# Optimization experiments

Measured on AMD Instinct MI355X. Metric: run time of the kernel, lower is better.

## Reference

```python
import jax, jax.numpy as jnp
import numpy as np

B, S, E, H, SHARE = 32, 1024, 256, 256, 2


def setup_inputs() -> dict:
    key = jax.random.key(0)
    ks = jax.random.split(key, 14)
    sc_e = 1.0 / np.sqrt(E)
    sc_h = 1.0 / np.sqrt(H)
    mk = lambda k, shape, sc: (jax.random.normal(k, shape, jnp.float32) * sc)
    return {
        "inputs": jax.random.normal(ks[0], (B, S, E), jnp.float32),
        "mask": jnp.ones((B, S), jnp.float32),
        # forward-direction cell params
        "Wx": mk(ks[1], (E, 4 * H), sc_e),
        "Wh": mk(ks[2], (H, 4 * H), sc_h),
        "Ws": mk(ks[3], (H, 4 * H), sc_h),
        "b": jnp.zeros((4 * H,), jnp.float32),
        "Wrx": mk(ks[4], (SHARE, E, H), sc_e),
        "Wrh": mk(ks[5], (SHARE, H, H), sc_h),
        "br": jnp.zeros((SHARE, H), jnp.float32),
        # reverse-direction cell params (deepcopy in torch; distinct draws here)
        "Wx_r": mk(ks[6], (E, 4 * H), sc_e),
        "Wh_r": mk(ks[7], (H, 4 * H), sc_h),
        "Ws_r": mk(ks[8], (H, 4 * H), sc_h),
        "b_r": jnp.zeros((4 * H,), jnp.float32),
        "Wrx_r": mk(ks[9], (SHARE, E, H), sc_e),
        "Wrh_r": mk(ks[10], (SHARE, H, H), sc_h),
        "br_r": jnp.zeros((SHARE, H), jnp.float32),
        "idx": 1,
    }


def _run_dir(xs, ms, params, idx, reverse):
    # xs: [S,B,E] time-major, ms: [S,B]
    Wx, Wh, Ws, b, Wrx, Wrh, br = params
    if reverse:
        xs = xs[::-1]
        ms = ms[::-1]
    Bt = xs.shape[1]
    Hd = Wh.shape[0]
    K = Wrx.shape[0]
    h0 = jnp.zeros((Bt, Hd), xs.dtype)
    c0 = jnp.zeros((Bt, Hd), xs.dtype)
    s0 = jnp.zeros((K, Bt, Hd), xs.dtype)  # shared cells (init_s)

    def step(carry, xm):
        h, c, s = carry
        x_t, m_t = xm
        # gates read x, h, and the idx-selected shared cell
        z = x_t @ Wx + h @ Wh + s[idx] @ Ws + b  # [B, 4H]
        i, f, g, o = jnp.split(z, 4, axis=-1)
        c_new = jax.nn.sigmoid(f) * c + jax.nn.sigmoid(i) * jnp.tanh(g)
        h_new = jax.nn.sigmoid(o) * jnp.tanh(c_new)
        m = m_t[:, None]
        h = m * h_new + (1.0 - m) * h
        c = m * c_new + (1.0 - m) * c
        # shared-cell gates, all K at once: [K,B,H]
        r = jax.nn.sigmoid(
            jnp.einsum("be,keh->kbh", x_t, Wrx)
            + jnp.einsum("bh,khj->kbj", h, Wrh)
            + br[:, None, :]
        )
        s_new = r * s + (1.0 - r) * c[None]
        s = m[None] * s_new + (1.0 - m[None]) * s
        return (h, c, s), (h, c, s)

    _, (hs, cs, ss) = jax.lax.scan(step, (h0, c0, s0), (xs, ms))
    if reverse:
        hs, cs, ss = hs[::-1], cs[::-1], ss[::-1]
    return hs, cs, ss  # [S,B,H], [S,B,H], [S,K,B,H]


def reference(inputs, mask, Wx, Wh, Ws, b, Wrx, Wrh, br,
              Wx_r, Wh_r, Ws_r, b_r, Wrx_r, Wrh_r, br_r, idx):
    xs = inputs.transpose(1, 0, 2)  # [S,B,E]
    ms = mask.T  # [S,B]
    hs_f, cs_f, ss_f = _run_dir(xs, ms, (Wx, Wh, Ws, b, Wrx, Wrh, br), idx, False)
    hs_r, cs_r, ss_r = _run_dir(xs, ms, (Wx_r, Wh_r, Ws_r, b_r, Wrx_r, Wrh_r, br_r), idx, True)
    h_f = jnp.concatenate([hs_f, hs_r], axis=-1)  # [S,B,2H]
    c_f = jnp.concatenate([cs_f, cs_r], axis=-1)  # [S,B,2H]
    # final_list: per shared-cell index, stacked over time -> [K,S,B,2H]
    s_f = jnp.concatenate([ss_f, ss_r], axis=-1).transpose(1, 0, 2, 3)
    return (h_f, c_f, s_f)
```

## Files before the change

### kernel.cpp

```cpp
#include <hip/hip_runtime.h>
#include <hip/hip_bf16.h>
#include <cstdint>
#include <cstddef>


typedef __bf16 bf16x8 __attribute__((ext_vector_type(8)));
typedef float  f32x4  __attribute__((ext_vector_type(4)));
typedef unsigned long long u64x2 __attribute__((ext_vector_type(2)));

#define DEVINL __device__ __forceinline__

constexpr int Ss = 1024;

constexpr size_t OFF_FLAGS = 0;
constexpr size_t OFF_H   = 1024;
constexpr size_t SZ_HS   = (size_t)2*2*32*512;
constexpr size_t OFF_S   = OFF_H + SZ_HS;
constexpr size_t OFF_WH  = OFF_S + SZ_HS;
constexpr size_t SZ_W    = (size_t)2*1024*256*2;
constexpr size_t OFF_WX  = OFF_WH + SZ_W;
constexpr size_t OFF_WS  = OFF_WX + SZ_W;
constexpr size_t OFF_WRX = OFF_WS + SZ_W;
constexpr size_t SZ_WR   = (size_t)2*2*256*256*2;
constexpr size_t OFF_WRH = OFF_WRX + SZ_WR;

DEVINL unsigned short f2bf(float f) {
    unsigned u = __builtin_bit_cast(unsigned, f);
    u += 0x7FFFu + ((u >> 16) & 1u);
    return (unsigned short)(u >> 16);
}
DEVINL unsigned long long pack4(float4 v) {
    return (unsigned long long)f2bf(v.x) | ((unsigned long long)f2bf(v.y) << 16)
         | ((unsigned long long)f2bf(v.z) << 32) | ((unsigned long long)f2bf(v.w) << 48);
}
DEVINL float sigm(float x) { return 1.f / (1.f + __expf(-x)); }

__global__ void prepass(const float* __restrict__ Wx0, const float* __restrict__ Wh0,
                        const float* __restrict__ Ws0,
                        const float* __restrict__ Wx1, const float* __restrict__ Wh1,
                        const float* __restrict__ Ws1,
                        const float* __restrict__ Wrx0, const float* __restrict__ Wrh0,
                        const float* __restrict__ Wrx1, const float* __restrict__ Wrh1,
                        unsigned char* __restrict__ ws)
{
    unsigned short* whT  = (unsigned short*)(ws + OFF_WH);
    unsigned short* wxT  = (unsigned short*)(ws + OFF_WX);
    unsigned short* wsT  = (unsigned short*)(ws + OFF_WS);
    unsigned short* wrxT = (unsigned short*)(ws + OFF_WRX);
    unsigned short* wrhT = (unsigned short*)(ws + OFF_WRH);
    int tid = blockIdx.x * blockDim.x + threadIdx.x;
    int NT  = gridDim.x * blockDim.x;
    for (int e = tid; e < 2*1024*256; e += NT) {
        int d = e >> 18, r = e & 262143, n = r >> 8, k = r & 255;
        whT[e] = f2bf((d ? Wh1 : Wh0)[k*1024 + n]);
        wxT[e] = f2bf((d ? Wx1 : Wx0)[k*1024 + n]);
        wsT[e] = f2bf((d ? Ws1 : Ws0)[k*1024 + n]);
    }
    for (int e = tid; e < 2*2*256*256; e += NT) {
        int d = e >> 17, r = e & 131071, kk = r >> 16, r2 = r & 65535;
        int j = r2 >> 8, k = r2 & 255;
        wrxT[e] = f2bf((d ? Wrx1 : Wrx0)[(kk*256 + k)*256 + j]);
        wrhT[e] = f2bf((d ? Wrh1 : Wrh0)[(kk*256 + k)*256 + j]);
    }
    if (blockIdx.x == 0 && threadIdx.x < 256) ((unsigned*)ws)[threadIdx.x] = 0u;
}

#define FRAG_PTR(Mt,kt,lqv,m) \
    ((unsigned long long*)(sA + (size_t)(((((Mt)*24+(kt))*4+(lqv))*16+(m))*8)))

__launch_bounds__(256, 1)
__global__ void bislstm(const float* __restrict__ inputs, const float* __restrict__ mask,
                        const float* __restrict__ b0,  const float* __restrict__ b1,
                        const float* __restrict__ br0, const float* __restrict__ br1,
                        const int* __restrict__ idxp,
                        unsigned char* __restrict__ ws, float* __restrict__ out)
{
    const int bid = blockIdx.x;
    const int d   = bid >> 5;
    const int g   = bid & 31;
    const int tid = threadIdx.x;
    const int wave = tid >> 6, lane = tid & 63;
    const int lm = lane & 15, lq = lane >> 4;

    __shared__ __align__(16) unsigned short sA[24576];
    __shared__ float zs[2][32][16];
    __shared__ float rsx[32][16], rsh[32][16];
    __shared__ float sC[32][8], sHs[32][8], sS2[2][32][8];
    __shared__ __align__(8) unsigned short sHb[256], sSb[256];

    const unsigned short* whT  = (const unsigned short*)(ws + OFF_WH)  + (size_t)d*1024*256;
    const unsigned short* wxT  = (const unsigned short*)(ws + OFF_WX)  + (size_t)d*1024*256;
    const unsigned short* wsT  = (const unsigned short*)(ws + OFF_WS)  + (size_t)d*1024*256;
    const unsigned short* wrxT = (const unsigned short*)(ws + OFF_WRX) + (size_t)d*2*256*256;
    const unsigned short* wrhT = (const unsigned short*)(ws + OFF_WRH) + (size_t)d*2*256*256;
    unsigned long long* Hbuf = (unsigned long long*)(ws + OFF_H);
    unsigned long long* Sbuf = (unsigned long long*)(ws + OFF_S);
    unsigned* flagsH = (unsigned*)ws + d*64;
    unsigned* flagsS = (unsigned*)ws + 128 + d*64;
    const int idxv = idxp[0];
    const float* bd  = d ? b1  : b0;
    const float* brd = d ? br1 : br0;

    const int zMt = wave & 1, zNt = wave >> 1;
    const int znl = zNt*16 + lm;
    const int zcol = (znl >> 3)*256 + g*8 + (znl & 7);
    const int rks = lm >> 3;
    const int rj  = g*8 + (lm & 7);

    bf16x8 whf[8], wsf[8], wxf[8], rwf[8];
#pragma unroll
    for (int kt = 0; kt < 8; ++kt) {
        whf[kt] = *(const bf16x8*)(whT + (size_t)zcol*256 + kt*32 + lq*8);
        wsf[kt] = *(const bf16x8*)(wsT + (size_t)zcol*256 + kt*32 + lq*8);
        wxf[kt] = *(const bf16x8*)(wxT + (size_t)zcol*256 + kt*32 + lq*8);
    }
    {
        const unsigned short* wrT = (wave < 2) ? wrxT : wrhT;
#pragma unroll
        for (int kt = 0; kt < 8; ++kt)
            rwf[kt] = *(const bf16x8*)(wrT + (size_t)(rks*256 + rj)*256 + kt*32 + lq*8);
    }

    {
        unsigned long long* z8 = (unsigned long long*)sA;
#pragma unroll
        for (int i = 0; i < 16; ++i) {
            int r = tid + 256*i;
            int u = (r & 2047) + (r >> 11)*3072;
            z8[u] = 0ULL;
        }
        int b_ = tid >> 3, j = tid & 7;
        sC[b_][j] = 0.f; sHs[b_][j] = 0.f; sS2[0][b_][j] = 0.f; sS2[1][b_][j] = 0.f;
    }
    {
        int tx0 = d ? (Ss - 1) : 0;
#pragma unroll
        for (int i = 0; i < 4; ++i) {
            int b_ = (tid & 7) + 8*i;
            int j  = tid >> 3;
            const float* xp = inputs + (((size_t)b_*Ss + tx0) << 8) + j*8;
            float4 v0 = *(const float4*)xp;
            float4 v1 = *(const float4*)(xp + 4);
            u64x2 pk; pk.x = pack4(v0); pk.y = pack4(v1);
            *(u64x2*)FRAG_PTR(b_ >> 4, 16 + (j >> 2), j & 3, b_ & 15) = pk;
        }
    }
    __syncthreads();

    const int eb = tid >> 3, ej = tid & 7;
    const int gj = g*8 + ej;
    const float bias_i = bd[gj], bias_f = bd[256+gj], bias_g = bd[512+gj], bias_o = bd[768+gj];
    const float brr0 = brd[gj], brr1 = brd[256+gj];

    const unsigned short* aBase = sA + (size_t)((zMt*96 + lq)*128 + lm*8);

    for (int t = 0; t < Ss; ++t) {
        const int tx = d ? (Ss - 1 - t) : t;
        const int pc = t & 1;
        const unsigned want = (unsigned)(t + 1);

        f32x4 acc = {0.f, 0.f, 0.f, 0.f};
#pragma unroll
        for (int kt = 0; kt < 8; ++kt)
            acc = __builtin_amdgcn_mfma_f32_16x16x32_bf16(*(const bf16x8*)(aBase + kt*512), whf[kt], acc, 0, 0, 0);
#pragma unroll
        for (int kt = 0; kt < 8; ++kt)
            acc = __builtin_amdgcn_mfma_f32_16x16x32_bf16(*(const bf16x8*)(aBase + (8+kt)*512), wsf[kt], acc, 0, 0, 0);
#pragma unroll
        for (int kt = 0; kt < 8; ++kt)
            acc = __builtin_amdgcn_mfma_f32_16x16x32_bf16(*(const bf16x8*)(aBase + (16+kt)*512), wxf[kt], acc, 0, 0, 0);
#pragma unroll
        for (int r = 0; r < 4; ++r)
            zs[zNt][zMt*16 + lq*4 + r][lm] = acc[r];
        __syncthreads();

        float m_, cu_, hu_;
        {
            float zi = zs[0][eb][ej]   + bias_i;
            float zf = zs[0][eb][8+ej] + bias_f;
            float zg = zs[1][eb][ej]   + bias_g;
            float zo = zs[1][eb][8+ej] + bias_o;
            float co = sC[eb][ej], ho = sHs[eb][ej];
            float cn = sigm(zf)*co + sigm(zi)*tanhf(zg);
            float hn = sigm(zo)*tanhf(cn);
            m_  = mask[(size_t)eb*Ss + tx];
            cu_ = m_*cn + (1.f - m_)*co;
            hu_ = m_*hn + (1.f - m_)*ho;
            sC[eb][ej] = cu_; sHs[eb][ej] = hu_;
            sHb[tid] = f2bf(hu_);
            out[((size_t)tx*32 + eb)*512 + d*256 + gj] = hu_;
            out[16777216 + ((size_t)tx*32 + eb)*512 + d*256 + gj] = cu_;
        }
        __syncthreads();

        if (wave == 0) {
            unsigned long long pk = *(const unsigned long long*)&sHb[lane*4];
            __hip_atomic_store(Hbuf + (size_t)(pc*2 + d)*2048 + (size_t)(lane>>1)*64 + g*2 + (lane&1),
                               pk, __ATOMIC_RELAXED, __HIP_MEMORY_SCOPE_AGENT);
            asm volatile("s_waitcnt vmcnt(0)" ::: "memory");
            if (lane == 0)
                __hip_atomic_store(flagsH + g, want, __ATOMIC_RELAXED, __HIP_MEMORY_SCOPE_AGENT);
        }
        if (wave < 2) {
            f32x4 ra = {0.f, 0.f, 0.f, 0.f};
#pragma unroll
            for (int kt = 0; kt < 8; ++kt)
                ra = __builtin_amdgcn_mfma_f32_16x16x32_bf16(*(const bf16x8*)(aBase + (16+kt)*512), rwf[kt], ra, 0, 0, 0);
#pragma unroll
            for (int r = 0; r < 4; ++r)
                rsx[zMt*16 + lq*4 + r][lm] = ra[r];
        } else if (wave == 3) {
            for (;;) {
                unsigned v = __hip_atomic_load(flagsH + (lane & 31), __ATOMIC_RELAXED, __HIP_MEMORY_SCOPE_AGENT);
                if (__ballot(v < want) == 0ULL) break;
                __builtin_amdgcn_s_sleep(1);
            }
            asm volatile("" ::: "memory");
        }
        __syncthreads();

        {
            unsigned long long* src = Hbuf + (size_t)(pc*2 + d)*2048;
#pragma unroll
            for (int i = 0; i < 4; ++i) {
                int b_ = (tid & 7) + 8*i;
                int j  = tid >> 3;
                unsigned long long v0 = __hip_atomic_load(src + (size_t)b_*64 + j*2,     __ATOMIC_RELAXED, __HIP_MEMORY_SCOPE_AGENT);
                unsigned long long v1 = __hip_atomic_load(src + (size_t)b_*64 + j*2 + 1, __ATOMIC_RELAXED, __HIP_MEMORY_SCOPE_AGENT);
                u64x2 pk; pk.x = v0; pk.y = v1;
                *(u64x2*)FRAG_PTR(b_ >> 4, (j >> 2), j & 3, b_ & 15) = pk;
            }
        }
        __syncthreads();

        if (wave >= 2) {
            f32x4 ra = {0.f, 0.f, 0.f, 0.f};
#pragma unroll
            for (int kt = 0; kt < 8; ++kt)
                ra = __builtin_amdgcn_mfma_f32_16x16x32_bf16(*(const bf16x8*)(aBase + kt*512), rwf[kt], ra, 0, 0, 0);
#pragma unroll
            for (int r = 0; r < 4; ++r)
                rsh[zMt*16 + lq*4 + r][lm] = ra[r];
        } else if (t + 1 < Ss) {
            int txn = d ? (Ss - 2 - t) : (t + 1);
#pragma unroll
            for (int i = 0; i < 8; ++i) {
                int b_ = (tid & 7) + 8*(i >> 1);
                int j  = (tid >> 3) + 16*(i & 1);
                const float* xp = inputs + (((size_t)b_*Ss + txn) << 8) + j*8;
                float4 v0 = *(const float4*)xp;
                float4 v1 = *(const float4*)(xp + 4);
                u64x2 pk; pk.x = pack4(v0); pk.y = pack4(v1);
                *(u64x2*)FRAG_PTR(b_ >> 4, 16 + (j >> 2), j & 3, b_ & 15) = pk;
            }
        }
        __syncthreads();

        {
#pragma unroll
            for (int kk = 0; kk < 2; ++kk) {
                float rv = rsx[eb][kk*8+ej] + rsh[eb][kk*8+ej] + (kk ? brr1 : brr0);
                float rr = sigm(rv);
                float so = sS2[kk][eb][ej];
                float sn = rr*so + (1.f - rr)*cu_;
                float su = m_*sn + (1.f - m_)*so;
                sS2[kk][eb][ej] = su;
                out[33554432 + (((size_t)kk*1024 + tx)*32 + eb)*512 + d*256 + gj] = su;
                if (kk == idxv) sSb[tid] = f2bf(su);
            }
        }
        __syncthreads();

        if (wave == 0) {
            unsigned long long pk = *(const unsigned long long*)&sSb[lane*4];
            __hip_atomic_store(Sbuf + (size_t)(pc*2 + d)*2048 + (size_t)(lane>>1)*64 + g*2 + (lane&1),
                               pk, __ATOMIC_RELAXED, __HIP_MEMORY_SCOPE_AGENT);
            asm volatile("s_waitcnt vmcnt(0)" ::: "memory");
            if (lane == 0)
                __hip_atomic_store(flagsS + g, want, __ATOMIC_RELAXED, __HIP_MEMORY_SCOPE_AGENT);
        } else if (wave == 3 && t + 1 < Ss) {
            for (;;) {
                unsigned v = __hip_atomic_load(flagsS + (lane & 31), __ATOMIC_RELAXED, __HIP_MEMORY_SCOPE_AGENT);
                if (__ballot(v < want) == 0ULL) break;
                __builtin_amdgcn_s_sleep(1);
            }
            asm volatile("" ::: "memory");
        }
        __syncthreads();

        if (t + 1 < Ss) {
            unsigned long long* src = Sbuf + (size_t)(pc*2 + d)*2048;
#pragma unroll
            for (int i = 0; i < 4; ++i) {
                int b_ = (tid & 7) + 8*i;
                int j  = tid >> 3;
                unsigned long long v0 = __hip_atomic_load(src + (size_t)b_*64 + j*2,     __ATOMIC_RELAXED, __HIP_MEMORY_SCOPE_AGENT);
                unsigned long long v1 = __hip_atomic_load(src + (size_t)b_*64 + j*2 + 1, __ATOMIC_RELAXED, __HIP_MEMORY_SCOPE_AGENT);
                u64x2 pk; pk.x = v0; pk.y = v1;
                *(u64x2*)FRAG_PTR(b_ >> 4, 8 + (j >> 2), j & 3, b_ & 15) = pk;
            }
            __syncthreads();
        }
    }
}

extern "C" void kernel_launch(void* const* d_in, const int* in_sizes, int n_in,
                              void* d_out, int out_size, void* d_ws, size_t ws_size,
                              hipStream_t stream) {
    const float* inputs = (const float*)d_in[0];
    const float* mask_  = (const float*)d_in[1];
    const float* Wx0  = (const float*)d_in[2];
    const float* Wh0  = (const float*)d_in[3];
    const float* Ws0  = (const float*)d_in[4];
    const float* b0   = (const float*)d_in[5];
    const float* Wrx0 = (const float*)d_in[6];
    const float* Wrh0 = (const float*)d_in[7];
    const float* br0  = (const float*)d_in[8];
    const float* Wx1  = (const float*)d_in[9];
    const float* Wh1  = (const float*)d_in[10];
    const float* Ws1  = (const float*)d_in[11];
    const float* b1   = (const float*)d_in[12];
    const float* Wrx1 = (const float*)d_in[13];
    const float* Wrh1 = (const float*)d_in[14];
    const float* br1  = (const float*)d_in[15];
    const int*   idxp = (const int*)d_in[16];
    unsigned char* ws = (unsigned char*)d_ws;

    hipLaunchKernelGGL(prepass, dim3(512), dim3(256), 0, stream,
                       Wx0, Wh0, Ws0, Wx1, Wh1, Ws1, Wrx0, Wrh0, Wrx1, Wrh1, ws);
    hipLaunchKernelGGL(bislstm, dim3(64), dim3(256), 0, stream,
                       inputs, mask_, b0, b1, br0, br1, idxp,
                       ws, (float*)d_out);
}
```

Before: 11.95 ms.

## Recompute idx shared cell redundantly per block to drop second grid barrier

Removes the second cross-block flag exchange per timestep. Each block now recomputes the full idx-selected shared-cell state for all hidden units, using h and c gathered from the other blocks plus a precomputed x-side r term published through the workspace. The input projection for the next step is moved ahead and overlapped with the barrier spin, and h, c and s state is kept in registers instead of shared memory. In exchange each block does much more MFMA work, holds a large extra weight tile in registers and adds global traffic for c and r.

```diff
diff --git a/kernel.cpp b/kernel.cpp
--- a/kernel.cpp
+++ b/kernel.cpp
@@ -15,14 +15,15 @@
 constexpr size_t OFF_FLAGS = 0;
 constexpr size_t OFF_H   = 1024;
 constexpr size_t SZ_HS   = (size_t)2*2*32*512;
-constexpr size_t OFF_S   = OFF_H + SZ_HS;
-constexpr size_t OFF_WH  = OFF_S + SZ_HS;
+constexpr size_t OFF_R   = OFF_H + SZ_HS;
+constexpr size_t OFF_WH  = OFF_R + SZ_HS;
 constexpr size_t SZ_W    = (size_t)2*1024*256*2;
 constexpr size_t OFF_WX  = OFF_WH + SZ_W;
 constexpr size_t OFF_WS  = OFF_WX + SZ_W;
 constexpr size_t OFF_WRX = OFF_WS + SZ_W;
 constexpr size_t SZ_WR   = (size_t)2*2*256*256*2;
 constexpr size_t OFF_WRH = OFF_WRX + SZ_WR;
+constexpr size_t OFF_C   = OFF_WRH + SZ_WR;
 
 DEVINL unsigned short f2bf(float f) {
     unsigned u = __builtin_bit_cast(unsigned, f);
@@ -66,7 +67,7 @@
 }
 
 #define FRAG_PTR(Mt,kt,lqv,m) \
-    ((unsigned long long*)(sA + (size_t)(((((Mt)*24+(kt))*4+(lqv))*16+(m))*8)))
+    ((unsigned long long*)(sA + (size_t)(((((Mt)*16+(kt))*4+(lqv))*16+(m))*8)))
 
 __launch_bounds__(256, 1)
 __global__ void bislstm(const float* __restrict__ inputs, const float* __restrict__ mask,
@@ -82,21 +83,22 @@
     const int wave = tid >> 6, lane = tid & 63;
     const int lm = lane & 15, lq = lane >> 4;
 
-    __shared__ __align__(16) unsigned short sA[24576];
+    __shared__ __align__(16) unsigned short sA[16384];
     __shared__ float zs[2][32][16];
-    __shared__ float rsx[32][16], rsh[32][16];
-    __shared__ float sC[32][8], sHs[32][8], sS2[2][32][8];
-    __shared__ __align__(8) unsigned short sHb[256], sSb[256];
+    __shared__ float rsxS[2][32][16];
+    __shared__ float rshS[32][16];
+    __shared__ float mL[32];
 
     const unsigned short* whT  = (const unsigned short*)(ws + OFF_WH)  + (size_t)d*1024*256;
     const unsigned short* wxT  = (const unsigned short*)(ws + OFF_WX)  + (size_t)d*1024*256;
     const unsigned short* wsT  = (const unsigned short*)(ws + OFF_WS)  + (size_t)d*1024*256;
     const unsigned short* wrxT = (const unsigned short*)(ws + OFF_WRX) + (size_t)d*2*256*256;
     const unsigned short* wrhT = (const unsigned short*)(ws + OFF_WRH) + (size_t)d*2*256*256;
-    unsigned long long* Hbuf = (unsigned long long*)(ws + OFF_H);
-    unsigned long long* Sbuf = (unsigned long long*)(ws + OFF_S);
-    unsigned* flagsH = (unsigned*)ws + d*64;
-    unsigned* flagsS = (unsigned*)ws + 128 + d*64;
+    unsigned long long* Hbuf  = (unsigned long long*)(ws + OFF_H);
+    unsigned short*     HbufS = (unsigned short*)(ws + OFF_H);
+    unsigned long long* Rbuf  = (unsigned long long*)(ws + OFF_R);
+    float*              CbufF = (float*)(ws + OFF_C);
+    unsigned* flags = (unsigned*)ws + d*64;
     const int idxv = idxp[0];
     const float* bd  = d ? b1  : b0;
     const float* brd = d ? br1 : br0;
@@ -107,7 +109,7 @@
     const int rks = lm >> 3;
     const int rj  = g*8 + (lm & 7);
 
-    bf16x8 whf[8], wsf[8], wxf[8], rwf[8];
+    bf16x8 whf[8], wsf[8], wxf[8], rwf[8], wbig[4][8];
 #pragma unroll
     for (int kt = 0; kt < 8; ++kt) {
         whf[kt] = *(const bf16x8*)(whT + (size_t)zcol*256 + kt*32 + lq*8);
@@ -115,34 +117,57 @@
         wxf[kt] = *(const bf16x8*)(wxT + (size_t)zcol*256 + kt*32 + lq*8);
     }
     {
-        const unsigned short* wrT = (wave < 2) ? wrxT : wrhT;
+        const unsigned short* wrT = (wave < 2) ? wrhT : wrxT;
 #pragma unroll
         for (int kt = 0; kt < 8; ++kt)
             rwf[kt] = *(const bf16x8*)(wrT + (size_t)(rks*256 + rj)*256 + kt*32 + lq*8);
     }
+    float brB[4]; bool ownN[4];
+#pragma unroll
+    for (int n = 0; n < 4; ++n) {
+        const int j16 = wave*64 + n*16 + lm;
+#pragma unroll
+        for (int kt = 0; kt < 8; ++kt)
+            wbig[n][kt] = *(const bf16x8*)(wrhT + (size_t)(idxv*256 + j16)*256 + kt*32 + lq*8);
+        brB[n]  = brd[idxv*256 + j16];
+        ownN[n] = ((j16 >> 3) == g);
+    }
 
     {
         unsigned long long* z8 = (unsigned long long*)sA;
 #pragma unroll
-        for (int i = 0; i < 16; ++i) {
-            int r = tid + 256*i;
-            int u = (r & 2047) + (r >> 11)*3072;
-            z8[u] = 0ULL;
-        }
-        int b_ = tid >> 3, j = tid & 7;
-        sC[b_][j] = 0.f; sHs[b_][j] = 0.f; sS2[0][b_][j] = 0.f; sS2[1][b_][j] = 0.f;
-    }
+        for (int i = 0; i < 16; ++i) z8[tid + 256*i] = 0ULL;
+    }
+
+    f32x4 zacc;
     {
-        int tx0 = d ? (Ss - 1) : 0;
-#pragma unroll
-        for (int i = 0; i < 4; ++i) {
-            int b_ = (tid & 7) + 8*i;
-            int j  = tid >> 3;
-            const float* xp = inputs + (((size_t)b_*Ss + tx0) << 8) + j*8;
-            float4 v0 = *(const float4*)xp;
-            float4 v1 = *(const float4*)(xp + 4);
+        const int tx0 = d ? (Ss - 1) : 0;
+        const float* xp = inputs + (((size_t)(zMt*16 + lm)*Ss + tx0) << 8) + lq*8;
+        bf16x8 xf[8];
+#pragma unroll
+        for (int kt = 0; kt < 8; ++kt) {
+            float4 v0 = *(const float4*)(xp + kt*32);
+            float4 v1 = *(const float4*)(xp + kt*32 + 4);
             u64x2 pk; pk.x = pack4(v0); pk.y = pack4(v1);
-            *(u64x2*)FRAG_PTR(b_ >> 4, 16 + (j >> 2), j & 3, b_ & 15) = pk;
+            xf[kt] = __builtin_bit_cast(bf16x8, pk);
+        }
+        f32x4 a = {0.f, 0.f, 0.f, 0.f};
+#pragma unroll
+        for (int kt = 0; kt < 8; ++kt)
+            a = __builtin_amdgcn_mfma_f32_16x16x32_bf16(xf[kt], wxf[kt], a, 0, 0, 0);
+        zacc = a;
+        if (wave >= 2) {
+            f32x4 ra = {0.f, 0.f, 0.f, 0.f};
+#pragma unroll
+            for (int kt = 0; kt < 8; ++kt)
+                ra = __builtin_amdgcn_mfma_f32_16x16x32_bf16(xf[kt], rwf[kt], ra, 0, 0, 0);
+#pragma unroll
+            for (int r = 0; r < 4; ++r) rsxS[0][zMt*16 + lq*4 + r][lm] = ra[r];
+            if (rks == idxv) {
+                float4 f4; f4.x = ra[0]; f4.y = ra[1]; f4.z = ra[2]; f4.w = ra[3];
+                __hip_atomic_store(Rbuf + (size_t)d*2048 + ((rj*32 + zMt*16 + lq*4) >> 2),
+                                   pack4(f4), __ATOMIC_RELAXED, __HIP_MEMORY_SCOPE_AGENT);
+            }
         }
     }
     __syncthreads();
@@ -151,27 +176,32 @@
     const int gj = g*8 + ej;
     const float bias_i = bd[gj], bias_f = bd[256+gj], bias_g = bd[512+gj], bias_o = bd[768+gj];
     const float brr0 = brd[gj], brr1 = brd[256+gj];
-
-    const unsigned short* aBase = sA + (size_t)((zMt*96 + lq)*128 + lm*8);
-
+    float hprev = 0.f, cprev = 0.f, s1prev = 0.f;
+    float sreg[2][4][4] = {};
+    unsigned long long cg[2][4][2], rg[2][4];
+
+    const unsigned short* aBase = sA + (size_t)(zMt*8192 + lq*128 + lm*8);
+
+#pragma unroll 1
     for (int t = 0; t < Ss; ++t) {
         const int tx = d ? (Ss - 1 - t) : t;
-        const int pc = t & 1;
+        const int pc = t & 1, pcn = pc ^ 1;
         const unsigned want = (unsigned)(t + 1);
-
-        f32x4 acc = {0.f, 0.f, 0.f, 0.f};
-#pragma unroll
-        for (int kt = 0; kt < 8; ++kt)
-            acc = __builtin_amdgcn_mfma_f32_16x16x32_bf16(*(const bf16x8*)(aBase + kt*512), whf[kt], acc, 0, 0, 0);
-#pragma unroll
-        for (int kt = 0; kt < 8; ++kt)
-            acc = __builtin_amdgcn_mfma_f32_16x16x32_bf16(*(const bf16x8*)(aBase + (8+kt)*512), wsf[kt], acc, 0, 0, 0);
-#pragma unroll
-        for (int kt = 0; kt < 8; ++kt)
-            acc = __builtin_amdgcn_mfma_f32_16x16x32_bf16(*(const bf16x8*)(aBase + (16+kt)*512), wxf[kt], acc, 0, 0, 0);
-#pragma unroll
-        for (int r = 0; r < 4; ++r)
-            zs[zNt][zMt*16 + lq*4 + r][lm] = acc[r];
+        const bool more = (t + 1 < Ss);
+
+        if (tid < 32) mL[tid] = mask[(size_t)tid*Ss + tx];
+        {
+            f32x4 acc = zacc;
+#pragma unroll
+            for (int kt = 0; kt < 8; ++kt)
+                acc = __builtin_amdgcn_mfma_f32_16x16x32_bf16(*(const bf16x8*)(aBase + kt*512), whf[kt], acc, 0, 0, 0);
+#pragma unroll
+            for (int kt = 0; kt < 8; ++kt)
+                acc = __builtin_amdgcn_mfma_f32_16x16x32_bf16(*(const bf16x8*)(aBase + (8+kt)*512), wsf[kt], acc, 0, 0, 0);
+#pragma unroll
+            for (int r = 0; r < 4; ++r)
+                zs[zNt][zMt*16 + lq*4 + r][lm] = acc[r];
+        }
         __syncthreads();
 
         float m_, cu_, hu_;
@@ -180,126 +210,143 @@
             float zf = zs[0][eb][8+ej] + bias_f;
             float zg = zs[1][eb][ej]   + bias_g;
             float zo = zs[1][eb][8+ej] + bias_o;
-            float co = sC[eb][ej], ho = sHs[eb][ej];
-            float cn = sigm(zf)*co + sigm(zi)*tanhf(zg);
+            float cn = sigm(zf)*cprev + sigm(zi)*tanhf(zg);
             float hn = sigm(zo)*tanhf(cn);
-            m_  = mask[(size_t)eb*Ss + tx];
-            cu_ = m_*cn + (1.f - m_)*co;
-            hu_ = m_*hn + (1.f - m_)*ho;
-            sC[eb][ej] = cu_; sHs[eb][ej] = hu_;
-            sHb[tid] = f2bf(hu_);
-            out[((size_t)tx*32 + eb)*512 + d*256 + gj] = hu_;
-            out[16777216 + ((size_t)tx*32 + eb)*512 + d*256 + gj] = cu_;
-        }
+            m_  = mL[eb];
+            cu_ = m_*cn + (1.f - m_)*cprev;
+            hu_ = m_*hn + (1.f - m_)*hprev;
+            cprev = cu_; hprev = hu_;
+            __hip_atomic_store(HbufS + (size_t)(pc*2 + d)*8192 + (size_t)eb*256 + gj,
+                               f2bf(hu_), __ATOMIC_RELAXED, __HIP_MEMORY_SCOPE_AGENT);
+            __hip_atomic_store(CbufF + (size_t)(pc*2 + d)*8192 + (size_t)gj*32 + eb,
+                               cu_, __ATOMIC_RELAXED, __HIP_MEMORY_SCOPE_AGENT);
+        }
+        asm volatile("s_waitcnt vmcnt(0)" ::: "memory");
         __syncthreads();
 
-        if (wave == 0) {
-            unsigned long long pk = *(const unsigned long long*)&sHb[lane*4];
-            __hip_atomic_store(Hbuf + (size_t)(pc*2 + d)*2048 + (size_t)(lane>>1)*64 + g*2 + (lane&1),
-                               pk, __ATOMIC_RELAXED, __HIP_MEMORY_SCOPE_AGENT);
-            asm volatile("s_waitcnt vmcnt(0)" ::: "memory");
-            if (lane == 0)
-                __hip_atomic_store(flagsH + g, want, __ATOMIC_RELAXED, __HIP_MEMORY_SCOPE_AGENT);
-        }
-        if (wave < 2) {
-            f32x4 ra = {0.f, 0.f, 0.f, 0.f};
-#pragma unroll
-            for (int kt = 0; kt < 8; ++kt)
-                ra = __builtin_amdgcn_mfma_f32_16x16x32_bf16(*(const bf16x8*)(aBase + (16+kt)*512), rwf[kt], ra, 0, 0, 0);
-#pragma unroll
-            for (int r = 0; r < 4; ++r)
-                rsx[zMt*16 + lq*4 + r][lm] = ra[r];
-        } else if (wave == 3) {
-            for (;;) {
-                unsigned v = __hip_atomic_load(flagsH + (lane & 31), __ATOMIC_RELAXED, __HIP_MEMORY_SCOPE_AGENT);
-                if (__ballot(v < want) == 0ULL) break;
-                __builtin_amdgcn_s_sleep(1);
-            }
-            asm volatile("" ::: "memory");
-        }
-        __syncthreads();
-
-        {
-            unsigned long long* src = Hbuf + (size_t)(pc*2 + d)*2048;
+        if (tid == 0)
+            __hip_atomic_store(flags + g, want, __ATOMIC_RELAXED, __HIP_MEMORY_SCOPE_AGENT);
+        out[((size_t)tx*32 + eb)*512 + d*256 + gj] = hu_;
+        out[16777216 + ((size_t)tx*32 + eb)*512 + d*256 + gj] = cu_;
+
+        bf16x8 xf[8];
+        if (more) {
+            const int txn = d ? (Ss - 2 - t) : (t + 1);
+            const float* xp = inputs + (((size_t)(zMt*16 + lm)*Ss + txn) << 8) + lq*8;
+#pragma unroll
+            for (int kt = 0; kt < 8; ++kt) {
+                float4 v0 = *(const float4*)(xp + kt*32);
+                float4 v1 = *(const float4*)(xp + kt*32 + 4);
+                u64x2 pk; pk.x = pack4(v0); pk.y = pack4(v1);
+                xf[kt] = __builtin_bit_cast(bf16x8, pk);
+            }
+        }
+        for (;;) {
+            unsigned v = __hip_atomic_load(flags + (lane & 31), __ATOMIC_RELAXED, __HIP_MEMORY_SCOPE_AGENT);
+            if (__ballot(v < want) == 0ULL) break;
+            __builtin_amdgcn_s_sleep(1);
+        }
+        asm volatile("" ::: "memory");
+        {
+            const unsigned long long* src = Hbuf + (size_t)(pc*2 + d)*2048;
 #pragma unroll
             for (int i = 0; i < 4; ++i) {
                 int b_ = (tid & 7) + 8*i;
-                int j  = tid >> 3;
-                unsigned long long v0 = __hip_atomic_load(src + (size_t)b_*64 + j*2,     __ATOMIC_RELAXED, __HIP_MEMORY_SCOPE_AGENT);
-                unsigned long long v1 = __hip_atomic_load(src + (size_t)b_*64 + j*2 + 1, __ATOMIC_RELAXED, __HIP_MEMORY_SCOPE_AGENT);
+                int jj = tid >> 3;
+                unsigned long long v0 = __hip_atomic_load(src + (size_t)b_*64 + jj*2,     __ATOMIC_RELAXED, __HIP_MEMORY_SCOPE_AGENT);
+                unsigned long long v1 = __hip_atomic_load(src + (size_t)b_*64 + jj*2 + 1, __ATOMIC_RELAXED, __HIP_MEMORY_SCOPE_AGENT);
                 u64x2 pk; pk.x = v0; pk.y = v1;
-                *(u64x2*)FRAG_PTR(b_ >> 4, (j >> 2), j & 3, b_ & 15) = pk;
+                *(u64x2*)FRAG_PTR(b_ >> 4, jj >> 2, jj & 3, b_ & 15) = pk;
+            }
+        }
+        {
+            const unsigned long long* Cb = (const unsigned long long*)(ws + OFF_C) + (size_t)(pc*2 + d)*4096;
+            const unsigned long long* Rb = (const unsigned long long*)(ws + OFF_R) + (size_t)(pc*2 + d)*2048;
+#pragma unroll
+            for (int Mt = 0; Mt < 2; ++Mt)
+#pragma unroll
+            for (int n = 0; n < 4; ++n) {
+                const int j16 = wave*64 + n*16 + lm;
+                const int b0  = Mt*16 + lq*4;
+                cg[Mt][n][0] = __hip_atomic_load(Cb + ((j16*32 + b0) >> 1),     __ATOMIC_RELAXED, __HIP_MEMORY_SCOPE_AGENT);
+                cg[Mt][n][1] = __hip_atomic_load(Cb + ((j16*32 + b0) >> 1) + 1, __ATOMIC_RELAXED, __HIP_MEMORY_SCOPE_AGENT);
+                rg[Mt][n]    = __hip_atomic_load(Rb + ((j16*32 + b0) >> 2),     __ATOMIC_RELAXED, __HIP_MEMORY_SCOPE_AGENT);
+            }
+        }
+        if (more) {
+            f32x4 a = {0.f, 0.f, 0.f, 0.f};
+#pragma unroll
+            for (int kt = 0; kt < 8; ++kt)
+                a = __builtin_amdgcn_mfma_f32_16x16x32_bf16(xf[kt], wxf[kt], a, 0, 0, 0);
+            zacc = a;
+            if (wave >= 2) {
+                f32x4 ra = {0.f, 0.f, 0.f, 0.f};
+#pragma unroll
+                for (int kt = 0; kt < 8; ++kt)
+                    ra = __builtin_amdgcn_mfma_f32_16x16x32_bf16(xf[kt], rwf[kt], ra, 0, 0, 0);
+#pragma unroll
+                for (int r = 0; r < 4; ++r) rsxS[pcn][zMt*16 + lq*4 + r][lm] = ra[r];
+                if (rks == idxv) {
+                    float4 f4; f4.x = ra[0]; f4.y = ra[1]; f4.z = ra[2]; f4.w = ra[3];
+                    __hip_atomic_store(Rbuf + (size_t)(pcn*2 + d)*2048 + ((rj*32 + zMt*16 + lq*4) >> 2),
+                                       pack4(f4), __ATOMIC_RELAXED, __HIP_MEMORY_SCOPE_AGENT);
+                }
             }
         }
         __syncthreads();
 
-        if (wave >= 2) {
-            f32x4 ra = {0.f, 0.f, 0.f, 0.f};
-#pragma unroll
-            for (int kt = 0; kt < 8; ++kt)
-                ra = __builtin_amdgcn_mfma_f32_16x16x32_bf16(*(const bf16x8*)(aBase + kt*512), rwf[kt], ra, 0, 0, 0);
-#pragma unroll
-            for (int r = 0; r < 4; ++r)
-                rsh[zMt*16 + lq*4 + r][lm] = ra[r];
-        } else if (t + 1 < Ss) {
-            int txn = d ? (Ss - 2 - t) : (t + 1);
-#pragma unroll
-            for (int i = 0; i < 8; ++i) {
-                int b_ = (tid & 7) + 8*(i >> 1);
-                int j  = (tid >> 3) + 16*(i & 1);
-                const float* xp = inputs + (((size_t)b_*Ss + txn) << 8) + j*8;
-                float4 v0 = *(const float4*)xp;
-                float4 v1 = *(const float4*)(xp + 4);
-                u64x2 pk; pk.x = pack4(v0); pk.y = pack4(v1);
-                *(u64x2*)FRAG_PTR(b_ >> 4, 16 + (j >> 2), j & 3, b_ & 15) = pk;
+#pragma unroll
+        for (int Mt = 0; Mt < 2; ++Mt) {
+            bf16x8 hf[8];
+#pragma unroll
+            for (int kt = 0; kt < 8; ++kt)
+                hf[kt] = *(const bf16x8*)(sA + (size_t)(Mt*8192 + kt*512 + lq*128 + lm*8));
+            float mrow[4];
+#pragma unroll
+            for (int r = 0; r < 4; ++r) mrow[r] = mL[Mt*16 + lq*4 + r];
+#pragma unroll
+            for (int n = 0; n < 4; ++n) {
+                f32x4 a = {0.f, 0.f, 0.f, 0.f};
+#pragma unroll
+                for (int kt = 0; kt < 8; ++kt)
+                    a = __builtin_amdgcn_mfma_f32_16x16x32_bf16(hf[kt], wbig[n][kt], a, 0, 0, 0);
+                const int j16 = wave*64 + n*16 + lm;
+                const int kts = 8 + wave*2 + (n >> 1);
+                const int lqs = (n*2 + (lm >> 3)) & 3;
+#pragma unroll
+                for (int r = 0; r < 4; ++r) {
+                    const int b = Mt*16 + lq*4 + r;
+                    float cv = __builtin_bit_cast(float, (unsigned)(cg[Mt][n][r >> 1] >> ((r & 1)*32)));
+                    float rx = __builtin_bit_cast(float, ((unsigned)(unsigned short)(rg[Mt][n] >> (r*16))) << 16);
+                    float rr = sigm(a[r] + rx + brB[n]);
+                    float so = sreg[Mt][n][r];
+                    float sn = rr*so + (1.f - rr)*cv;
+                    float su = mrow[r]*sn + (1.f - mrow[r])*so;
+                    sreg[Mt][n][r] = su;
+                    sA[(size_t)(Mt*8192 + kts*512 + lqs*128 + (b & 15)*8 + (lm & 7))] = f2bf(su);
+                    if (ownN[n])
+                        out[33554432 + (((size_t)idxv*1024 + tx)*32 + b)*512 + d*256 + j16] = su;
+                }
+            }
+            if (wave < 2 && Mt == zMt) {
+                f32x4 ra = {0.f, 0.f, 0.f, 0.f};
+#pragma unroll
+                for (int kt = 0; kt < 8; ++kt)
+                    ra = __builtin_amdgcn_mfma_f32_16x16x32_bf16(hf[kt], rwf[kt], ra, 0, 0, 0);
+#pragma unroll
+                for (int r = 0; r < 4; ++r) rshS[zMt*16 + lq*4 + r][lm] = ra[r];
             }
         }
         __syncthreads();
 
         {
-#pragma unroll
-            for (int kk = 0; kk < 2; ++kk) {
-                float rv = rsx[eb][kk*8+ej] + rsh[eb][kk*8+ej] + (kk ? brr1 : brr0);
-                float rr = sigm(rv);
-                float so = sS2[kk][eb][ej];
-                float sn = rr*so + (1.f - rr)*cu_;
-                float su = m_*sn + (1.f - m_)*so;
-                sS2[kk][eb][ej] = su;
-                out[33554432 + (((size_t)kk*1024 + tx)*32 + eb)*512 + d*256 + gj] = su;
-                if (kk == idxv) sSb[tid] = f2bf(su);
-            }
-        }
-        __syncthreads();
-
-        if (wave == 0) {
-            unsigned long long pk = *(const unsigned long long*)&sSb[lane*4];
-            __hip_atomic_store(Sbuf + (size_t)(pc*2 + d)*2048 + (size_t)(lane>>1)*64 + g*2 + (lane&1),
-                               pk, __ATOMIC_RELAXED, __HIP_MEMORY_SCOPE_AGENT);
-            asm volatile("s_waitcnt vmcnt(0)" ::: "memory");
-            if (lane == 0)
-                __hip_atomic_store(flagsS + g, want, __ATOMIC_RELAXED, __HIP_MEMORY_SCOPE_AGENT);
-        } else if (wave == 3 && t + 1 < Ss) {
-            for (;;) {
-                unsigned v = __hip_atomic_load(flagsS + (lane & 31), __ATOMIC_RELAXED, __HIP_MEMORY_SCOPE_AGENT);
-                if (__ballot(v < want) == 0ULL) break;
-                __builtin_amdgcn_s_sleep(1);
-            }
-            asm volatile("" ::: "memory");
-        }
-        __syncthreads();
-
-        if (t + 1 < Ss) {
-            unsigned long long* src = Sbuf + (size_t)(pc*2 + d)*2048;
-#pragma unroll
-            for (int i = 0; i < 4; ++i) {
-                int b_ = (tid & 7) + 8*i;
-                int j  = tid >> 3;
-                unsigned long long v0 = __hip_atomic_load(src + (size_t)b_*64 + j*2,     __ATOMIC_RELAXED, __HIP_MEMORY_SCOPE_AGENT);
-                unsigned long long v1 = __hip_atomic_load(src + (size_t)b_*64 + j*2 + 1, __ATOMIC_RELAXED, __HIP_MEMORY_SCOPE_AGENT);
-                u64x2 pk; pk.x = v0; pk.y = v1;
-                *(u64x2*)FRAG_PTR(b_ >> 4, 8 + (j >> 2), j & 3, b_ & 15) = pk;
-            }
-            __syncthreads();
+            const int k1 = 1 - idxv;
+            float rv = rsxS[pc][eb][k1*8 + ej] + rshS[eb][k1*8 + ej] + (k1 ? brr1 : brr0);
+            float rr = sigm(rv);
+            float sn = rr*s1prev + (1.f - rr)*cu_;
+            float su = m_*sn + (1.f - m_)*s1prev;
+            s1prev = su;
+            out[33554432 + (((size_t)k1*1024 + tx)*32 + eb)*512 + d*256 + gj] = su;
         }
     }
 }
```

Result: slower. 15.26 ms (+27.7%).
